# Performance work log

Measured on AMD Instinct MI355X. Metric: run time of the kernel, lower is better.

The kernel has to match this reference:

```python
import jax, jax.numpy as jnp
import numpy as np

N = 100000
E = 1600000
D = 128
H = 128


def gcn_conv(x, W, b, src, dst, n_nodes):
    # x: [N, Din] -> linear transform first (PyG GCNConv)
    h = x @ W  # [N, Dout]
    # add self loops
    loop = jnp.arange(n_nodes, dtype=src.dtype)
    s = jnp.concatenate([src, loop])
    d = jnp.concatenate([dst, loop])
    # symmetric normalization: deg computed on destination (col) with unit weights
    deg = jnp.zeros((n_nodes,), dtype=h.dtype).at[d].add(1.0)
    dinv = jnp.where(deg > 0, jax.lax.rsqrt(deg), 0.0)
    norm = dinv[s] * dinv[d]  # [E+N]
    msg = h[s] * norm[:, None]  # gather + scale
    out = jax.ops.segment_sum(msg, d, num_segments=n_nodes)
    return out + b


def setup_inputs() -> dict:
    key = jax.random.key(0)
    ks = jax.random.split(key, 8)
    x = jax.random.normal(ks[0], (N, D), dtype=jnp.float32)
    edge_index = jax.random.randint(ks[1], (2, E), 0, N, dtype=jnp.int32)
    sc = 1.0 / np.sqrt(D)
    gate_W = jax.random.uniform(ks[2], (D, D), jnp.float32, -sc, sc)
    gate_b = jax.random.uniform(ks[3], (D,), jnp.float32, -sc, sc)
    W1 = jax.random.normal(ks[4], (D, H), dtype=jnp.float32) * sc
    b1 = jnp.zeros((H,), jnp.float32)
    W2 = jax.random.normal(ks[5], (H, H), dtype=jnp.float32) * (1.0 / np.sqrt(H))
    b2 = jnp.zeros((H,), jnp.float32)
    return {"x": x, "edge_index": edge_index, "gate_W": gate_W, "gate_b": gate_b,
            "W1": W1, "b1": b1, "W2": W2, "b2": b2}


def reference(x, edge_index, gate_W, gate_b, W1, b1, W2, b2):
    src, dst = edge_index[0], edge_index[1]
    gate = jax.nn.sigmoid(x @ gate_W + gate_b)
    h = x * gate
    h = gcn_conv(h, W1, b1, src, dst, N)
    h = jax.nn.relu(h)
    h = gcn_conv(h, W2, b2, src, dst, N)
    return h
```

## Files before the change

### kernel.cpp

```cpp
#include <hip/hip_runtime.h>
#include <hip/hip_bf16.h>
#include <math.h>


#define BUCKET_SHIFT 8
#define BUCKET_W 256
#define CAP 4864
#define NB_MAX 512
#define OSTRIDE 136

typedef __attribute__((ext_vector_type(8))) short bf16x8;
typedef __attribute__((ext_vector_type(4))) float f32x4;

__device__ __forceinline__ unsigned short f2bf(float x) {
    unsigned int u = __float_as_uint(x);
    unsigned int r = (u + 0x7FFFu + ((u >> 16) & 1u)) >> 16;
    return (unsigned short)r;
}
__device__ __forceinline__ float blo(unsigned int u) { return __uint_as_float(u << 16); }
__device__ __forceinline__ float bhi(unsigned int u) { return __uint_as_float(u & 0xFFFF0000u); }

__device__ __forceinline__ void cvt_hilo8(const float* v, bf16x8& hi, bf16x8& lo) {
#pragma unroll
    for (int j = 0; j < 8; j++) {
        unsigned short h = f2bf(v[j]);
        float hf = __uint_as_float((unsigned int)h << 16);
        hi[j] = (short)h;
        lo[j] = (short)f2bf(v[j] - hf);
    }
}

__device__ __forceinline__ f32x4 MF(bf16x8 a, bf16x8 b, f32x4 c) {
    return __builtin_amdgcn_mfma_f32_16x16x32_bf16(a, b, c, 0, 0, 0);
}

__global__ void partition_kernel(const int* __restrict__ src, const int* __restrict__ dst,
                                 int* __restrict__ bucketCursor, unsigned int* __restrict__ part,
                                 int E, int NB, int chunk) {
    __shared__ int hist[NB_MAX];
    __shared__ int basec[NB_MAX];
    int t = threadIdx.x;
    int b = blockIdx.x;
    int e0 = b * chunk;
    int e1 = min(E, e0 + chunk);

    for (int i = t; i < NB; i += 256) hist[i] = 0;
    __syncthreads();
    for (int e = e0 + t; e < e1; e += 256) {
        int bb = dst[e] >> BUCKET_SHIFT;
        atomicAdd(&hist[bb], 1);
    }
    __syncthreads();
    for (int i = t; i < NB; i += 256) {
        int c = hist[i];
        basec[i] = c ? atomicAdd(&bucketCursor[i], c) : 0;
    }
    __syncthreads();
    for (int i = t; i < NB; i += 256) hist[i] = 0;
    __syncthreads();
    for (int e = e0 + t; e < e1; e += 256) {
        int d = dst[e], s = src[e];
        int bb = d >> BUCKET_SHIFT;
        int r = atomicAdd(&hist[bb], 1);
        int pos = basec[bb] + r;
        if (pos < CAP)
            part[(size_t)bb * CAP + pos] = ((unsigned int)(d & (BUCKET_W - 1)) << 17) | (unsigned int)s;
    }
}

__global__ void bucket_scan_kernel(const int* __restrict__ bucketCursor,
                                   int* __restrict__ bucketBase, int NB) {
    __shared__ int sm[NB_MAX];
    int t = threadIdx.x;
    int v = (t < NB) ? min(bucketCursor[t], CAP) : 0;
    sm[t] = v;
    __syncthreads();
    for (int off = 1; off < NB_MAX; off <<= 1) {
        int a = (t >= off) ? sm[t - off] : 0;
        __syncthreads();
        sm[t] += a;
        __syncthreads();
    }
    if (t < NB) bucketBase[t + 1] = sm[t];
    if (t == 0) bucketBase[0] = 0;
}

__launch_bounds__(256, 2)
__global__ void bucket_fill_kernel(const unsigned int* __restrict__ part,
                                   const int* __restrict__ bucketBase,
                                   int* __restrict__ rowptr, float* __restrict__ dinv,
                                   int* __restrict__ col, int N) {
    __shared__ unsigned int eLDS[CAP];
    __shared__ int deg[BUCKET_W];
    __shared__ int cur[BUCKET_W];
    __shared__ int wsum[4];

    int b = blockIdx.x, t = threadIdx.x;
    int base = bucketBase[b];
    int cnt = bucketBase[b + 1] - base;

    for (int i = t; i < cnt; i += 256) eLDS[i] = part[(size_t)b * CAP + i];
    deg[t] = 0;
    __syncthreads();
    for (int i = t; i < cnt; i += 256) atomicAdd(&deg[eLDS[i] >> 17], 1);
    __syncthreads();

    int v = deg[t];
    int incl = v;
    int lane = t & 63, w = t >> 6;
    for (int off = 1; off < 64; off <<= 1) {
        int u = __shfl_up(incl, off, 64);
        if (lane >= off) incl += u;
    }
    if (lane == 63) wsum[w] = incl;
    __syncthreads();
    int add = 0;
#pragma unroll
    for (int j = 0; j < 4; j++) if (j < w) add += wsum[j];
    int excl = add + incl - v;
    cur[t] = excl;

    int gnode = b * BUCKET_W + t;
    if (gnode < N) {
        rowptr[gnode] = base + excl;
        dinv[gnode] = rsqrtf((float)(v + 1));
    }
    if (b == gridDim.x - 1 && t == 0) rowptr[N] = base + cnt;
    __syncthreads();

    for (int i = t; i < cnt; i += 256) {
        unsigned int ev = eLDS[i];
        int dl = ev >> 17;
        int p = atomicAdd(&cur[dl], 1);
        col[base + p] = (int)(ev & 0x1FFFFu);
    }
}

__global__ void prep_weights_kernel(const float* __restrict__ W0, const float* __restrict__ W1,
                                    const float* __restrict__ W2, uint4* __restrict__ img) {
    int idx = blockIdx.x * 256 + threadIdx.x;
    int c = idx & 127, kb = (idx >> 7) & 15, w = idx >> 11;
    const float* W = (w == 0) ? W0 : (w == 1) ? W1 : W2;
    bf16x8 hb;
#pragma unroll
    for (int j = 0; j < 8; j++) hb[j] = (short)f2bf(W[(size_t)(kb * 8 + j) * 128 + c]);
    img[w * 2048 + c * 16 + (kb ^ (c & 15))] = *(uint4*)&hb;
}

__global__ __launch_bounds__(512)
void gate_kernel(const float* __restrict__ x, const uint4* __restrict__ gimg,
                 const float* __restrict__ gate_b, unsigned short* __restrict__ hpack,
                 int n) {
    __shared__ uint4 Wl[2048];
    __shared__ unsigned short OutS[128 * OSTRIDE];

    int t = threadIdx.x;
    int lane = t & 63, wv = t >> 6;
    int blockRow = blockIdx.x * 128;

    for (int idx = t; idx < 2048; idx += 512) Wl[idx] = gimg[idx];

    bf16x8 Ahi[4], Alo[4];
    {
        int arow = blockRow + wv * 16 + (lane & 15);
        const float* ap = x + (size_t)min(arow, n - 1) * 128 + (lane >> 4) * 8;
#pragma unroll
        for (int s = 0; s < 4; s++) {
            float v[8];
            *(float4*)&v[0] = *(const float4*)&ap[s * 32];
            *(float4*)&v[4] = *(const float4*)&ap[s * 32 + 4];
            cvt_hilo8(v, Ahi[s], Alo[s]);
        }
    }
    __syncthreads();

    f32x4 acc[8];
#pragma unroll
    for (int nt = 0; nt < 8; nt++) acc[nt] = (f32x4)(0.f);
#pragma unroll
    for (int s = 0; s < 4; s++) {
        int kb = s * 4 + (lane >> 4);
#pragma unroll
        for (int nt = 0; nt < 8; nt++) {
            int c = nt * 16 + (lane & 15);
            bf16x8 bh = *(bf16x8*)&Wl[c * 16 + (kb ^ (lane & 15))];
            acc[nt] = MF(Ahi[s], bh, acc[nt]);
            acc[nt] = MF(Alo[s], bh, acc[nt]);
        }
    }

    int rl0 = wv * 16 + (lane >> 4) * 4;
#pragma unroll
    for (int nt = 0; nt < 8; nt++) {
        int c = nt * 16 + (lane & 15);
        float gb = gate_b[c];
#pragma unroll
        for (int r = 0; r < 4; r++) {
            int grow = min(blockRow + rl0 + r, n - 1);
            float xv = x[(size_t)grow * 128 + c];
            float hv = xv / (1.f + __expf(-(acc[nt][r] + gb)));
            OutS[(rl0 + r) * OSTRIDE + c] = f2bf(hv);
        }
    }
    __syncthreads();
    {
        int row = t >> 2;
        int c0 = (t & 3) * 32;
        int grow = blockRow + row;
        if (grow < n) {
#pragma unroll
            for (int j = 0; j < 4; j++) {
                uint4 v = *(uint4*)&OutS[row * OSTRIDE + c0 + j * 8];
                *(uint4*)&hpack[(size_t)grow * 128 + c0 + j * 8] = v;
            }
        }
    }
}

__global__ __launch_bounds__(512)
void gemm_bf16_kernel(const unsigned short* __restrict__ A, const uint4* __restrict__ wimg,
                      const float* __restrict__ dinv, unsigned short* __restrict__ g,
                      int n) {
    __shared__ uint4 Wl[2048];
    __shared__ unsigned short OutS[128 * OSTRIDE];

    int t = threadIdx.x;
    int lane = t & 63, wv = t >> 6;
    int blockRow = blockIdx.x * 128;

    for (int idx = t; idx < 2048; idx += 512) Wl[idx] = wimg[idx];

    bf16x8 Af[4];
    {
        int arow = blockRow + wv * 16 + (lane & 15);
        const uint4* ap = (const uint4*)(A + (size_t)min(arow, n - 1) * 128);
#pragma unroll
        for (int s = 0; s < 4; s++) {
            uint4 u = ap[(lane >> 4) + s * 4];
            Af[s] = *(bf16x8*)&u;
        }
    }
    __syncthreads();

    f32x4 acc[8];
#pragma unroll
    for (int nt = 0; nt < 8; nt++) acc[nt] = (f32x4)(0.f);
#pragma unroll
    for (int s = 0; s < 4; s++) {
        int kb = s * 4 + (lane >> 4);
#pragma unroll
        for (int nt = 0; nt < 8; nt++) {
            int c = nt * 16 + (lane & 15);
            bf16x8 bh = *(bf16x8*)&Wl[c * 16 + (kb ^ (lane & 15))];
            acc[nt] = MF(Af[s], bh, acc[nt]);
        }
    }

    int rl0 = wv * 16 + (lane >> 4) * 4;
    float di[4];
#pragma unroll
    for (int r = 0; r < 4; r++) di[r] = dinv[min(blockRow + rl0 + r, n - 1)];
#pragma unroll
    for (int nt = 0; nt < 8; nt++) {
        int c = nt * 16 + (lane & 15);
#pragma unroll
        for (int r = 0; r < 4; r++)
            OutS[(rl0 + r) * OSTRIDE + c] = f2bf(acc[nt][r] * di[r]);
    }
    __syncthreads();
    {
        int row = t >> 2;
        int c0 = (t & 3) * 32;
        int grow = blockRow + row;
        if (grow < n) {
#pragma unroll
            for (int j = 0; j < 4; j++) {
                uint4 v = *(uint4*)&OutS[row * OSTRIDE + c0 + j * 8];
                *(uint4*)&g[(size_t)grow * 128 + c0 + j * 8] = v;
            }
        }
    }
}

template <int RELU, int PACK>
__global__ void spmm_kernel(const uint4* __restrict__ g16, const int* __restrict__ rowptr,
                            const int* __restrict__ col, const float* __restrict__ dinv,
                            const float* __restrict__ bias, void* __restrict__ outv,
                            int n) {
    int grp = threadIdx.x >> 4;
    int i = blockIdx.x * 16 + grp;
    if (i >= n) return;
    int c = threadIdx.x & 15;

    float acc[8];
    uint4 sv = g16[(size_t)i * 16 + c];
    acc[0] = blo(sv.x); acc[1] = bhi(sv.x);
    acc[2] = blo(sv.y); acc[3] = bhi(sv.y);
    acc[4] = blo(sv.z); acc[5] = bhi(sv.z);
    acc[6] = blo(sv.w); acc[7] = bhi(sv.w);

    int e0 = rowptr[i], e1 = rowptr[i + 1];
    int e = e0;
    for (; e + 4 <= e1; e += 4) {
        int s0 = col[e], s1 = col[e + 1], s2 = col[e + 2], s3 = col[e + 3];
        uint4 v0 = g16[(size_t)s0 * 16 + c];
        uint4 v1 = g16[(size_t)s1 * 16 + c];
        uint4 v2 = g16[(size_t)s2 * 16 + c];
        uint4 v3 = g16[(size_t)s3 * 16 + c];
        acc[0] += (blo(v0.x) + blo(v1.x)) + (blo(v2.x) + blo(v3.x));
        acc[1] += (bhi(v0.x) + bhi(v1.x)) + (bhi(v2.x) + bhi(v3.x));
        acc[2] += (blo(v0.y) + blo(v1.y)) + (blo(v2.y) + blo(v3.y));
        acc[3] += (bhi(v0.y) + bhi(v1.y)) + (bhi(v2.y) + bhi(v3.y));
        acc[4] += (blo(v0.z) + blo(v1.z)) + (blo(v2.z) + blo(v3.z));
        acc[5] += (bhi(v0.z) + bhi(v1.z)) + (bhi(v2.z) + bhi(v3.z));
        acc[6] += (blo(v0.w) + blo(v1.w)) + (blo(v2.w) + blo(v3.w));
        acc[7] += (bhi(v0.w) + bhi(v1.w)) + (bhi(v2.w) + bhi(v3.w));
    }
    for (; e < e1; e++) {
        int s0 = col[e];
        uint4 v0 = g16[(size_t)s0 * 16 + c];
        acc[0] += blo(v0.x); acc[1] += bhi(v0.x);
        acc[2] += blo(v0.y); acc[3] += bhi(v0.y);
        acc[4] += blo(v0.z); acc[5] += bhi(v0.z);
        acc[6] += blo(v0.w); acc[7] += bhi(v0.w);
    }

    float di = dinv[i];
    const float4* b4 = (const float4*)bias;
    float4 bv0 = b4[c * 2], bv1 = b4[c * 2 + 1];
    float r0[8];
    r0[0] = fmaf(acc[0], di, bv0.x);
    r0[1] = fmaf(acc[1], di, bv0.y);
    r0[2] = fmaf(acc[2], di, bv0.z);
    r0[3] = fmaf(acc[3], di, bv0.w);
    r0[4] = fmaf(acc[4], di, bv1.x);
    r0[5] = fmaf(acc[5], di, bv1.y);
    r0[6] = fmaf(acc[6], di, bv1.z);
    r0[7] = fmaf(acc[7], di, bv1.w);
    if (RELU) {
#pragma unroll
        for (int j = 0; j < 8; j++) r0[j] = fmaxf(r0[j], 0.f);
    }
    if (PACK) {
        ushort4 q0, q1;
        q0.x = f2bf(r0[0]); q0.y = f2bf(r0[1]); q0.z = f2bf(r0[2]); q0.w = f2bf(r0[3]);
        q1.x = f2bf(r0[4]); q1.y = f2bf(r0[5]); q1.z = f2bf(r0[6]); q1.w = f2bf(r0[7]);
        unsigned short* o = (unsigned short*)outv + (size_t)i * 128 + c * 8;
        *(ushort4*)&o[0] = q0;
        *(ushort4*)&o[4] = q1;
    } else {
        float* o = (float*)outv + (size_t)i * 128 + c * 8;
        *(float4*)&o[0] = *(float4*)&r0[0];
        *(float4*)&o[4] = *(float4*)&r0[4];
    }
}

extern "C" void kernel_launch(void* const* d_in, const int* in_sizes, int n_in,
                              void* d_out, int out_size, void* d_ws, size_t ws_size,
                              hipStream_t stream) {
    const float* x      = (const float*)d_in[0];
    const int*   ei     = (const int*)d_in[1];
    const float* gate_W = (const float*)d_in[2];
    const float* gate_b = (const float*)d_in[3];
    const float* W1     = (const float*)d_in[4];
    const float* b1     = (const float*)d_in[5];
    const float* W2     = (const float*)d_in[6];
    const float* b2     = (const float*)d_in[7];
    float* out = (float*)d_out;

    const int N = in_sizes[0] / 128;
    const int E = in_sizes[1] / 2;
    const int* src = ei;
    const int* dst = ei + E;
    const int NB = (N + BUCKET_W - 1) / BUCKET_W;

    char* p = (char*)d_ws;
    auto alloc = [&](size_t bytes) { char* q = p; p += (bytes + 255) & ~(size_t)255; return q; };
    int*   rowptr  = (int*)alloc(((size_t)N + 1) * 4);
    float* dinv    = (float*)alloc((size_t)N * 4);
    int*   colb    = (int*)alloc((size_t)E * 4);
    int*   bcursor = (int*)alloc((size_t)NB * 4);
    int*   bbase   = (int*)alloc(((size_t)NB + 1) * 4);
    uint4* wimg    = (uint4*)alloc((size_t)3 * 2048 * 16);
    unsigned int*   part    = (unsigned int*)alloc((size_t)NB * CAP * 4);
    unsigned short* hpack   = (unsigned short*)alloc((size_t)N * 128 * 2);
    unsigned short* g16     = (unsigned short*)alloc((size_t)N * 128 * 2);
    unsigned short* h1pack  = (unsigned short*)alloc((size_t)N * 128 * 2);

    prep_weights_kernel<<<24, 256, 0, stream>>>(gate_W, W1, W2, wimg);
    hipMemsetAsync(bcursor, 0, (size_t)NB * 4, stream);
    const int pblocks = 256;
    const int chunk = (E + pblocks - 1) / pblocks;
    partition_kernel<<<pblocks, 256, 0, stream>>>(src, dst, bcursor, part, E, NB, chunk);
    bucket_scan_kernel<<<1, NB_MAX, 0, stream>>>(bcursor, bbase, NB);
    bucket_fill_kernel<<<NB, 256, 0, stream>>>(part, bbase, rowptr, dinv, colb, N);

    int gblocks = (N + 127) / 128;
    int sblocks = (N + 15) / 16;
    gate_kernel<<<gblocks, 512, 0, stream>>>(x, wimg, gate_b, hpack, N);
    gemm_bf16_kernel<<<gblocks, 512, 0, stream>>>(hpack, wimg + 2048, dinv, g16, N);
    spmm_kernel<1, 1><<<sblocks, 256, 0, stream>>>((const uint4*)g16, rowptr, colb,
                                                   dinv, b1, h1pack, N);
    gemm_bf16_kernel<<<gblocks, 512, 0, stream>>>(h1pack, wimg + 4096, dinv, g16, N);
    spmm_kernel<0, 0><<<sblocks, 256, 0, stream>>>((const uint4*)g16, rowptr, colb,
                                                   dinv, b2, out, N);
}
```

Before: 245.6 us.

## Fuse graph-build stages with dense GEMMs and split SpMM columns into halves

Merges independent stages into shared launches. Weight prep and the cursor zeroing become one kernel, partition runs alongside the gate GEMM in one grid, and bucket fill runs alongside the first GCN GEMM in one grid. To allow that overlap, the first GEMM no longer applies dinv, and the first SpMM multiplies by dinv[src] per edge instead. Both SpMMs now split the 128 feature columns into two 64-column halves handled by separate blocks, and the final output uses nontemporal stores. This cuts launch count and serialisation, and lets graph construction overlap with dense work, at the cost of extra per-edge dinv loads and larger 512-thread blocks in the fill stage.

```diff
diff --git a/kernel.cpp b/kernel.cpp
--- a/kernel.cpp
+++ b/kernel.cpp
@@ -34,31 +34,50 @@
     return __builtin_amdgcn_mfma_f32_16x16x32_bf16(a, b, c, 0, 0, 0);
 }
 
-__global__ void partition_kernel(const int* __restrict__ src, const int* __restrict__ dst,
-                                 int* __restrict__ bucketCursor, unsigned int* __restrict__ part,
-                                 int E, int NB, int chunk) {
-    __shared__ int hist[NB_MAX];
-    __shared__ int basec[NB_MAX];
-    int t = threadIdx.x;
-    int b = blockIdx.x;
+__global__ __launch_bounds__(512)
+void prepinit_kernel(const float* __restrict__ W0, const float* __restrict__ W1,
+                     const float* __restrict__ W2, uint4* __restrict__ img,
+                     int* __restrict__ bcursor, int NB) {
+    int b = blockIdx.x, t = threadIdx.x;
+    if (b < 12) {
+        int idx = b * 512 + t;
+        int c = idx & 127, kb = (idx >> 7) & 15, w = idx >> 11;
+        const float* W = (w == 0) ? W0 : (w == 1) ? W1 : W2;
+        bf16x8 hb;
+#pragma unroll
+        for (int j = 0; j < 8; j++) hb[j] = (short)f2bf(W[(size_t)(kb * 8 + j) * 128 + c]);
+        img[w * 2048 + c * 16 + (kb ^ (c & 15))] = *(uint4*)&hb;
+    } else {
+        if (t < NB) bcursor[t] = 0;
+    }
+}
+
+__device__ __forceinline__ void partition_body(char* smem, int b, int t,
+                                               const int* __restrict__ src,
+                                               const int* __restrict__ dst,
+                                               int* __restrict__ bucketCursor,
+                                               unsigned int* __restrict__ part,
+                                               int E, int NB, int chunk) {
+    int* hist  = (int*)smem;
+    int* basec = hist + NB_MAX;
     int e0 = b * chunk;
     int e1 = min(E, e0 + chunk);
 
-    for (int i = t; i < NB; i += 256) hist[i] = 0;
-    __syncthreads();
-    for (int e = e0 + t; e < e1; e += 256) {
+    for (int i = t; i < NB; i += 512) hist[i] = 0;
+    __syncthreads();
+    for (int e = e0 + t; e < e1; e += 512) {
         int bb = dst[e] >> BUCKET_SHIFT;
         atomicAdd(&hist[bb], 1);
     }
     __syncthreads();
-    for (int i = t; i < NB; i += 256) {
+    for (int i = t; i < NB; i += 512) {
         int c = hist[i];
         basec[i] = c ? atomicAdd(&bucketCursor[i], c) : 0;
     }
     __syncthreads();
-    for (int i = t; i < NB; i += 256) hist[i] = 0;
-    __syncthreads();
-    for (int e = e0 + t; e < e1; e += 256) {
+    for (int i = t; i < NB; i += 512) hist[i] = 0;
+    __syncthreads();
+    for (int e = e0 + t; e < e1; e += 512) {
         int d = dst[e], s = src[e];
         int bb = d >> BUCKET_SHIFT;
         int r = atomicAdd(&hist[bb], 1);
@@ -68,8 +87,90 @@
     }
 }
 
-__global__ void bucket_scan_kernel(const int* __restrict__ bucketCursor,
-                                   int* __restrict__ bucketBase, int NB) {
+__device__ __forceinline__ void gate_body(char* smem, int gb, int t,
+                                          const float* __restrict__ x,
+                                          const uint4* __restrict__ gimg,
+                                          const float* __restrict__ gate_b,
+                                          unsigned short* __restrict__ hpack, int n) {
+    uint4* Wl = (uint4*)smem;
+    unsigned short* OutS = (unsigned short*)(smem + 32768);
+    int lane = t & 63, wv = t >> 6;
+    int blockRow = gb * 128;
+
+    for (int idx = t; idx < 2048; idx += 512) Wl[idx] = gimg[idx];
+
+    bf16x8 Ahi[4], Alo[4];
+    {
+        int arow = blockRow + wv * 16 + (lane & 15);
+        const float* ap = x + (size_t)min(arow, n - 1) * 128 + (lane >> 4) * 8;
+#pragma unroll
+        for (int s = 0; s < 4; s++) {
+            float v[8];
+            *(float4*)&v[0] = *(const float4*)&ap[s * 32];
+            *(float4*)&v[4] = *(const float4*)&ap[s * 32 + 4];
+            cvt_hilo8(v, Ahi[s], Alo[s]);
+        }
+    }
+    __syncthreads();
+
+    f32x4 acc[8];
+#pragma unroll
+    for (int nt = 0; nt < 8; nt++) acc[nt] = (f32x4)(0.f);
+#pragma unroll
+    for (int s = 0; s < 4; s++) {
+        int kb = s * 4 + (lane >> 4);
+#pragma unroll
+        for (int nt = 0; nt < 8; nt++) {
+            int c = nt * 16 + (lane & 15);
+            bf16x8 bh = *(bf16x8*)&Wl[c * 16 + (kb ^ (lane & 15))];
+            acc[nt] = MF(Ahi[s], bh, acc[nt]);
+            acc[nt] = MF(Alo[s], bh, acc[nt]);
+        }
+    }
+
+    int rl0 = wv * 16 + (lane >> 4) * 4;
+#pragma unroll
+    for (int nt = 0; nt < 8; nt++) {
+        int c = nt * 16 + (lane & 15);
+        float gb2 = gate_b[c];
+#pragma unroll
+        for (int r = 0; r < 4; r++) {
+            int grow = min(blockRow + rl0 + r, n - 1);
+            float xv = x[(size_t)grow * 128 + c];
+            float hv = xv / (1.f + __expf(-(acc[nt][r] + gb2)));
+            OutS[(rl0 + r) * OSTRIDE + c] = f2bf(hv);
+        }
+    }
+    __syncthreads();
+    {
+        int row = t >> 2;
+        int c0 = (t & 3) * 32;
+        int grow = blockRow + row;
+        if (grow < n) {
+#pragma unroll
+            for (int j = 0; j < 4; j++) {
+                uint4 v = *(uint4*)&OutS[row * OSTRIDE + c0 + j * 8];
+                *(uint4*)&hpack[(size_t)grow * 128 + c0 + j * 8] = v;
+            }
+        }
+    }
+}
+
+__global__ __launch_bounds__(512)
+void pg_kernel(const int* __restrict__ src, const int* __restrict__ dst,
+               int* __restrict__ bucketCursor, unsigned int* __restrict__ part,
+               int E, int NB, int chunk,
+               const float* __restrict__ x, const uint4* __restrict__ gimg,
+               const float* __restrict__ gate_b, unsigned short* __restrict__ hpack, int n) {
+    __shared__ __align__(16) char smem[67584];
+    int b = blockIdx.x, t = threadIdx.x;
+    if (b < 256) partition_body(smem, b, t, src, dst, bucketCursor, part, E, NB, chunk);
+    else         gate_body(smem, b - 256, t, x, gimg, gate_b, hpack, n);
+}
+
+__global__ __launch_bounds__(512)
+void bucket_scan_kernel(const int* __restrict__ bucketCursor,
+                        int* __restrict__ bucketBase, int NB) {
     __shared__ int sm[NB_MAX];
     int t = threadIdx.x;
     int v = (t < NB) ? min(bucketCursor[t], CAP) : 0;
@@ -85,27 +186,26 @@
     if (t == 0) bucketBase[0] = 0;
 }
 
-__launch_bounds__(256, 2)
-__global__ void bucket_fill_kernel(const unsigned int* __restrict__ part,
-                                   const int* __restrict__ bucketBase,
-                                   int* __restrict__ rowptr, float* __restrict__ dinv,
-                                   int* __restrict__ col, int N) {
-    __shared__ unsigned int eLDS[CAP];
-    __shared__ int deg[BUCKET_W];
-    __shared__ int cur[BUCKET_W];
-    __shared__ int wsum[4];
-
-    int b = blockIdx.x, t = threadIdx.x;
+__device__ __forceinline__ void fill_body(char* smem, int b, int t,
+                                          const unsigned int* __restrict__ part,
+                                          const int* __restrict__ bucketBase,
+                                          int* __restrict__ rowptr, float* __restrict__ dinv,
+                                          int* __restrict__ col, int N, int NB) {
+    unsigned int* eLDS = (unsigned int*)smem;
+    int* deg  = (int*)(smem + CAP * 4);
+    int* cur  = deg + BUCKET_W;
+    int* wsum = cur + BUCKET_W;
+
     int base = bucketBase[b];
     int cnt = bucketBase[b + 1] - base;
 
-    for (int i = t; i < cnt; i += 256) eLDS[i] = part[(size_t)b * CAP + i];
-    deg[t] = 0;
-    __syncthreads();
-    for (int i = t; i < cnt; i += 256) atomicAdd(&deg[eLDS[i] >> 17], 1);
-    __syncthreads();
-
-    int v = deg[t];
+    for (int i = t; i < cnt; i += 512) eLDS[i] = part[(size_t)b * CAP + i];
+    if (t < 256) deg[t] = 0;
+    __syncthreads();
+    for (int i = t; i < cnt; i += 512) atomicAdd(&deg[eLDS[i] >> 17], 1);
+    __syncthreads();
+
+    int v = (t < 256) ? deg[t] : 0;
     int incl = v;
     int lane = t & 63, w = t >> 6;
     for (int off = 1; off < 64; off <<= 1) {
@@ -118,17 +218,18 @@
 #pragma unroll
     for (int j = 0; j < 4; j++) if (j < w) add += wsum[j];
     int excl = add + incl - v;
-    cur[t] = excl;
-
-    int gnode = b * BUCKET_W + t;
-    if (gnode < N) {
-        rowptr[gnode] = base + excl;
-        dinv[gnode] = rsqrtf((float)(v + 1));
-    }
-    if (b == gridDim.x - 1 && t == 0) rowptr[N] = base + cnt;
-    __syncthreads();
-
-    for (int i = t; i < cnt; i += 256) {
+    if (t < 256) {
+        cur[t] = excl;
+        int gnode = b * BUCKET_W + t;
+        if (gnode < N) {
+            rowptr[gnode] = base + excl;
+            dinv[gnode] = rsqrtf((float)(v + 1));
+        }
+    }
+    if (b == NB - 1 && t == 0) rowptr[N] = base + cnt;
+    __syncthreads();
+
+    for (int i = t; i < cnt; i += 512) {
         unsigned int ev = eLDS[i];
         int dl = ev >> 17;
         int p = atomicAdd(&cur[dl], 1);
@@ -136,40 +237,27 @@
     }
 }
 
-__global__ void prep_weights_kernel(const float* __restrict__ W0, const float* __restrict__ W1,
-                                    const float* __restrict__ W2, uint4* __restrict__ img) {
-    int idx = blockIdx.x * 256 + threadIdx.x;
-    int c = idx & 127, kb = (idx >> 7) & 15, w = idx >> 11;
-    const float* W = (w == 0) ? W0 : (w == 1) ? W1 : W2;
-    bf16x8 hb;
-#pragma unroll
-    for (int j = 0; j < 8; j++) hb[j] = (short)f2bf(W[(size_t)(kb * 8 + j) * 128 + c]);
-    img[w * 2048 + c * 16 + (kb ^ (c & 15))] = *(uint4*)&hb;
-}
-
-__global__ __launch_bounds__(512)
-void gate_kernel(const float* __restrict__ x, const uint4* __restrict__ gimg,
-                 const float* __restrict__ gate_b, unsigned short* __restrict__ hpack,
-                 int n) {
-    __shared__ uint4 Wl[2048];
-    __shared__ unsigned short OutS[128 * OSTRIDE];
-
-    int t = threadIdx.x;
+template <int SCALE>
+__device__ __forceinline__ void gemm_body(char* smem, int gb, int t,
+                                          const unsigned short* __restrict__ A,
+                                          const uint4* __restrict__ wimg,
+                                          const float* __restrict__ dinv,
+                                          unsigned short* __restrict__ g, int n) {
+    uint4* Wl = (uint4*)smem;
+    unsigned short* OutS = (unsigned short*)(smem + 32768);
     int lane = t & 63, wv = t >> 6;
-    int blockRow = blockIdx.x * 128;
-
-    for (int idx = t; idx < 2048; idx += 512) Wl[idx] = gimg[idx];
-
-    bf16x8 Ahi[4], Alo[4];
+    int blockRow = gb * 128;
+
+    for (int idx = t; idx < 2048; idx += 512) Wl[idx] = wimg[idx];
+
+    bf16x8 Af[4];
     {
         int arow = blockRow + wv * 16 + (lane & 15);
-        const float* ap = x + (size_t)min(arow, n - 1) * 128 + (lane >> 4) * 8;
+        const uint4* ap = (const uint4*)(A + (size_t)min(arow, n - 1) * 128);
 #pragma unroll
         for (int s = 0; s < 4; s++) {
-            float v[8];
-            *(float4*)&v[0] = *(const float4*)&ap[s * 32];
-            *(float4*)&v[4] = *(const float4*)&ap[s * 32 + 4];
-            cvt_hilo8(v, Ahi[s], Alo[s]);
+            uint4 u = ap[(lane >> 4) + s * 4];
+            Af[s] = *(bf16x8*)&u;
         }
     }
     __syncthreads();
@@ -184,23 +272,21 @@
         for (int nt = 0; nt < 8; nt++) {
             int c = nt * 16 + (lane & 15);
             bf16x8 bh = *(bf16x8*)&Wl[c * 16 + (kb ^ (lane & 15))];
-            acc[nt] = MF(Ahi[s], bh, acc[nt]);
-            acc[nt] = MF(Alo[s], bh, acc[nt]);
+            acc[nt] = MF(Af[s], bh, acc[nt]);
         }
     }
 
     int rl0 = wv * 16 + (lane >> 4) * 4;
+    float di[4];
+#pragma unroll
+    for (int r = 0; r < 4; r++)
+        di[r] = SCALE ? dinv[min(blockRow + rl0 + r, n - 1)] : 1.f;
 #pragma unroll
     for (int nt = 0; nt < 8; nt++) {
         int c = nt * 16 + (lane & 15);
-        float gb = gate_b[c];
-#pragma unroll
-        for (int r = 0; r < 4; r++) {
-            int grow = min(blockRow + rl0 + r, n - 1);
-            float xv = x[(size_t)grow * 128 + c];
-            float hv = xv / (1.f + __expf(-(acc[nt][r] + gb)));
-            OutS[(rl0 + r) * OSTRIDE + c] = f2bf(hv);
-        }
+#pragma unroll
+        for (int r = 0; r < 4; r++)
+            OutS[(rl0 + r) * OSTRIDE + c] = f2bf(acc[nt][r] * di[r]);
     }
     __syncthreads();
     {
@@ -211,122 +297,84 @@
 #pragma unroll
             for (int j = 0; j < 4; j++) {
                 uint4 v = *(uint4*)&OutS[row * OSTRIDE + c0 + j * 8];
-                *(uint4*)&hpack[(size_t)grow * 128 + c0 + j * 8] = v;
+                *(uint4*)&g[(size_t)grow * 128 + c0 + j * 8] = v;
             }
         }
     }
+}
+
+__global__ __launch_bounds__(512)
+void fg_kernel(const unsigned int* __restrict__ part, const int* __restrict__ bucketBase,
+               int* __restrict__ rowptr, float* __restrict__ dinv, int* __restrict__ col,
+               int N, int NB,
+               const unsigned short* __restrict__ A, const uint4* __restrict__ wimg,
+               unsigned short* __restrict__ g) {
+    __shared__ __align__(16) char smem[67584];
+    int b = blockIdx.x, t = threadIdx.x;
+    if (b < NB) fill_body(smem, b, t, part, bucketBase, rowptr, dinv, col, N, NB);
+    else        gemm_body<0>(smem, b - NB, t, A, wimg, (const float*)nullptr, g, N);
 }
 
 __global__ __launch_bounds__(512)
 void gemm_bf16_kernel(const unsigned short* __restrict__ A, const uint4* __restrict__ wimg,
-                      const float* __restrict__ dinv, unsigned short* __restrict__ g,
-                      int n) {
-    __shared__ uint4 Wl[2048];
-    __shared__ unsigned short OutS[128 * OSTRIDE];
-
-    int t = threadIdx.x;
-    int lane = t & 63, wv = t >> 6;
-    int blockRow = blockIdx.x * 128;
-
-    for (int idx = t; idx < 2048; idx += 512) Wl[idx] = wimg[idx];
-
-    bf16x8 Af[4];
-    {
-        int arow = blockRow + wv * 16 + (lane & 15);
-        const uint4* ap = (const uint4*)(A + (size_t)min(arow, n - 1) * 128);
-#pragma unroll
-        for (int s = 0; s < 4; s++) {
-            uint4 u = ap[(lane >> 4) + s * 4];
-            Af[s] = *(bf16x8*)&u;
-        }
-    }
-    __syncthreads();
-
-    f32x4 acc[8];
-#pragma unroll
-    for (int nt = 0; nt < 8; nt++) acc[nt] = (f32x4)(0.f);
-#pragma unroll
-    for (int s = 0; s < 4; s++) {
-        int kb = s * 4 + (lane >> 4);
-#pragma unroll
-        for (int nt = 0; nt < 8; nt++) {
-            int c = nt * 16 + (lane & 15);
-            bf16x8 bh = *(bf16x8*)&Wl[c * 16 + (kb ^ (lane & 15))];
-            acc[nt] = MF(Af[s], bh, acc[nt]);
-        }
-    }
-
-    int rl0 = wv * 16 + (lane >> 4) * 4;
-    float di[4];
-#pragma unroll
-    for (int r = 0; r < 4; r++) di[r] = dinv[min(blockRow + rl0 + r, n - 1)];
-#pragma unroll
-    for (int nt = 0; nt < 8; nt++) {
-        int c = nt * 16 + (lane & 15);
-#pragma unroll
-        for (int r = 0; r < 4; r++)
-            OutS[(rl0 + r) * OSTRIDE + c] = f2bf(acc[nt][r] * di[r]);
-    }
-    __syncthreads();
-    {
-        int row = t >> 2;
-        int c0 = (t & 3) * 32;
-        int grow = blockRow + row;
-        if (grow < n) {
-#pragma unroll
-            for (int j = 0; j < 4; j++) {
-                uint4 v = *(uint4*)&OutS[row * OSTRIDE + c0 + j * 8];
-                *(uint4*)&g[(size_t)grow * 128 + c0 + j * 8] = v;
-            }
-        }
-    }
-}
-
-template <int RELU, int PACK>
+                      const float* __restrict__ dinv, unsigned short* __restrict__ g, int n) {
+    __shared__ __align__(16) char smem[67584];
+    gemm_body<1>(smem, blockIdx.x, threadIdx.x, A, wimg, dinv, g, n);
+}
+
+template <int RELU, int PACK, int DVSRC>
 __global__ void spmm_kernel(const uint4* __restrict__ g16, const int* __restrict__ rowptr,
                             const int* __restrict__ col, const float* __restrict__ dinv,
                             const float* __restrict__ bias, void* __restrict__ outv,
-                            int n) {
-    int grp = threadIdx.x >> 4;
-    int i = blockIdx.x * 16 + grp;
+                            int n, int nhb) {
+    int half = (blockIdx.x >= nhb) ? 1 : 0;
+    int rb = blockIdx.x - half * nhb;
+    int i = rb * 32 + (threadIdx.x >> 3);
     if (i >= n) return;
-    int c = threadIdx.x & 15;
-
+    int c = threadIdx.x & 7;
+
+    float di = dinv[i];
+    const uint4* gp = g16 + half * 8 + c;
     float acc[8];
-    uint4 sv = g16[(size_t)i * 16 + c];
-    acc[0] = blo(sv.x); acc[1] = bhi(sv.x);
-    acc[2] = blo(sv.y); acc[3] = bhi(sv.y);
-    acc[4] = blo(sv.z); acc[5] = bhi(sv.z);
-    acc[6] = blo(sv.w); acc[7] = bhi(sv.w);
+    uint4 sv = gp[(size_t)i * 16];
+    float wi = DVSRC ? di : 1.f;
+    acc[0] = wi * blo(sv.x); acc[1] = wi * bhi(sv.x);
+    acc[2] = wi * blo(sv.y); acc[3] = wi * bhi(sv.y);
+    acc[4] = wi * blo(sv.z); acc[5] = wi * bhi(sv.z);
+    acc[6] = wi * blo(sv.w); acc[7] = wi * bhi(sv.w);
 
     int e0 = rowptr[i], e1 = rowptr[i + 1];
     int e = e0;
     for (; e + 4 <= e1; e += 4) {
         int s0 = col[e], s1 = col[e + 1], s2 = col[e + 2], s3 = col[e + 3];
-        uint4 v0 = g16[(size_t)s0 * 16 + c];
-        uint4 v1 = g16[(size_t)s1 * 16 + c];
-        uint4 v2 = g16[(size_t)s2 * 16 + c];
-        uint4 v3 = g16[(size_t)s3 * 16 + c];
-        acc[0] += (blo(v0.x) + blo(v1.x)) + (blo(v2.x) + blo(v3.x));
-        acc[1] += (bhi(v0.x) + bhi(v1.x)) + (bhi(v2.x) + bhi(v3.x));
-        acc[2] += (blo(v0.y) + blo(v1.y)) + (blo(v2.y) + blo(v3.y));
-        acc[3] += (bhi(v0.y) + bhi(v1.y)) + (bhi(v2.y) + bhi(v3.y));
-        acc[4] += (blo(v0.z) + blo(v1.z)) + (blo(v2.z) + blo(v3.z));
-        acc[5] += (bhi(v0.z) + bhi(v1.z)) + (bhi(v2.z) + bhi(v3.z));
-        acc[6] += (blo(v0.w) + blo(v1.w)) + (blo(v2.w) + blo(v3.w));
-        acc[7] += (bhi(v0.w) + bhi(v1.w)) + (bhi(v2.w) + bhi(v3.w));
+        uint4 v0 = gp[(size_t)s0 * 16];
+        uint4 v1 = gp[(size_t)s1 * 16];
+        uint4 v2 = gp[(size_t)s2 * 16];
+        uint4 v3 = gp[(size_t)s3 * 16];
+        float w0 = DVSRC ? dinv[s0] : 1.f;
+        float w1 = DVSRC ? dinv[s1] : 1.f;
+        float w2 = DVSRC ? dinv[s2] : 1.f;
+        float w3 = DVSRC ? dinv[s3] : 1.f;
+        acc[0] = fmaf(w0, blo(v0.x), fmaf(w1, blo(v1.x), fmaf(w2, blo(v2.x), fmaf(w3, blo(v3.x), acc[0]))));
+        acc[1] = fmaf(w0, bhi(v0.x), fmaf(w1, bhi(v1.x), fmaf(w2, bhi(v2.x), fmaf(w3, bhi(v3.x), acc[1]))));
+        acc[2] = fmaf(w0, blo(v0.y), fmaf(w1, blo(v1.y), fmaf(w2, blo(v2.y), fmaf(w3, blo(v3.y), acc[2]))));
+        acc[3] = fmaf(w0, bhi(v0.y), fmaf(w1, bhi(v1.y), fmaf(w2, bhi(v2.y), fmaf(w3, bhi(v3.y), acc[3]))));
+        acc[4] = fmaf(w0, blo(v0.z), fmaf(w1, blo(v1.z), fmaf(w2, blo(v2.z), fmaf(w3, blo(v3.z), acc[4]))));
+        acc[5] = fmaf(w0, bhi(v0.z), fmaf(w1, bhi(v1.z), fmaf(w2, bhi(v2.z), fmaf(w3, bhi(v3.z), acc[5]))));
+        acc[6] = fmaf(w0, blo(v0.w), fmaf(w1, blo(v1.w), fmaf(w2, blo(v2.w), fmaf(w3, blo(v3.w), acc[6]))));
+        acc[7] = fmaf(w0, bhi(v0.w), fmaf(w1, bhi(v1.w), fmaf(w2, bhi(v2.w), fmaf(w3, bhi(v3.w), acc[7]))));
     }
     for (; e < e1; e++) {
         int s0 = col[e];
-        uint4 v0 = g16[(size_t)s0 * 16 + c];
-        acc[0] += blo(v0.x); acc[1] += bhi(v0.x);
-        acc[2] += blo(v0.y); acc[3] += bhi(v0.y);
-        acc[4] += blo(v0.z); acc[5] += bhi(v0.z);
-        acc[6] += blo(v0.w); acc[7] += bhi(v0.w);
-    }
-
-    float di = dinv[i];
-    const float4* b4 = (const float4*)bias;
+        uint4 v0 = gp[(size_t)s0 * 16];
+        float w0 = DVSRC ? dinv[s0] : 1.f;
+        acc[0] = fmaf(w0, blo(v0.x), acc[0]); acc[1] = fmaf(w0, bhi(v0.x), acc[1]);
+        acc[2] = fmaf(w0, blo(v0.y), acc[2]); acc[3] = fmaf(w0, bhi(v0.y), acc[3]);
+        acc[4] = fmaf(w0, blo(v0.z), acc[4]); acc[5] = fmaf(w0, bhi(v0.z), acc[5]);
+        acc[6] = fmaf(w0, blo(v0.w), acc[6]); acc[7] = fmaf(w0, bhi(v0.w), acc[7]);
+    }
+
+    const float4* b4 = (const float4*)(bias + half * 64);
     float4 bv0 = b4[c * 2], bv1 = b4[c * 2 + 1];
     float r0[8];
     r0[0] = fmaf(acc[0], di, bv0.x);
@@ -342,16 +390,18 @@
         for (int j = 0; j < 8; j++) r0[j] = fmaxf(r0[j], 0.f);
     }
     if (PACK) {
-        ushort4 q0, q1;
-        q0.x = f2bf(r0[0]); q0.y = f2bf(r0[1]); q0.z = f2bf(r0[2]); q0.w = f2bf(r0[3]);
-        q1.x = f2bf(r0[4]); q1.y = f2bf(r0[5]); q1.z = f2bf(r0[6]); q1.w = f2bf(r0[7]);
-        unsigned short* o = (unsigned short*)outv + (size_t)i * 128 + c * 8;
-        *(ushort4*)&o[0] = q0;
-        *(ushort4*)&o[4] = q1;
+        uint4 w;
+        w.x = (unsigned int)f2bf(r0[0]) | ((unsigned int)f2bf(r0[1]) << 16);
+        w.y = (unsigned int)f2bf(r0[2]) | ((unsigned int)f2bf(r0[3]) << 16);
+        w.z = (unsigned int)f2bf(r0[4]) | ((unsigned int)f2bf(r0[5]) << 16);
+        w.w = (unsigned int)f2bf(r0[6]) | ((unsigned int)f2bf(r0[7]) << 16);
+        *(uint4*)((unsigned short*)outv + (size_t)i * 128 + half * 64 + c * 8) = w;
     } else {
-        float* o = (float*)outv + (size_t)i * 128 + c * 8;
-        *(float4*)&o[0] = *(float4*)&r0[0];
-        *(float4*)&o[4] = *(float4*)&r0[4];
+        float* o = (float*)outv + (size_t)i * 128 + half * 64 + c * 8;
+        f32x4 a = *(f32x4*)&r0[0];
+        f32x4 b = *(f32x4*)&r0[4];
+        __builtin_nontemporal_store(a, (f32x4*)o);
+        __builtin_nontemporal_store(b, (f32x4*)(o + 4));
     }
 }
 
@@ -382,26 +432,25 @@
     int*   bcursor = (int*)alloc((size_t)NB * 4);
     int*   bbase   = (int*)alloc(((size_t)NB + 1) * 4);
     uint4* wimg    = (uint4*)alloc((size_t)3 * 2048 * 16);
-    unsigned int*   part    = (unsigned int*)alloc((size_t)NB * CAP * 4);
-    unsigned short* hpack   = (unsigned short*)alloc((size_t)N * 128 * 2);
-    unsigned short* g16     = (unsigned short*)alloc((size_t)N * 128 * 2);
-    unsigned short* h1pack  = (unsigned short*)alloc((size_t)N * 128 * 2);
-
-    prep_weights_kernel<<<24, 256, 0, stream>>>(gate_W, W1, W2, wimg);
-    hipMemsetAsync(bcursor, 0, (size_t)NB * 4, stream);
+    unsigned int*   part   = (unsigned int*)alloc((size_t)NB * CAP * 4);
+    unsigned short* hpack  = (unsigned short*)alloc((size_t)N * 128 * 2);
+    unsigned short* g16    = (unsigned short*)alloc((size_t)N * 128 * 2);
+    unsigned short* h1pack = (unsigned short*)alloc((size_t)N * 128 * 2);
+
     const int pblocks = 256;
     const int chunk = (E + pblocks - 1) / pblocks;
-    partition_kernel<<<pblocks, 256, 0, stream>>>(src, dst, bcursor, part, E, NB, chunk);
-    bucket_scan_kernel<<<1, NB_MAX, 0, stream>>>(bcursor, bbase, NB);
-    bucket_fill_kernel<<<NB, 256, 0, stream>>>(part, bbase, rowptr, dinv, colb, N);
-
     int gblocks = (N + 127) / 128;
-    int sblocks = (N + 15) / 16;
-    gate_kernel<<<gblocks, 512, 0, stream>>>(x, wimg, gate_b, hpack, N);
-    gemm_bf16_kernel<<<gblocks, 512, 0, stream>>>(hpack, wimg + 2048, dinv, g16, N);
-    spmm_kernel<1, 1><<<sblocks, 256, 0, stream>>>((const uint4*)g16, rowptr, colb,
-                                                   dinv, b1, h1pack, N);
+    int nhb = (N + 31) / 32;
+
+    prepinit_kernel<<<13, 512, 0, stream>>>(gate_W, W1, W2, wimg, bcursor, NB);
+    pg_kernel<<<256 + gblocks, 512, 0, stream>>>(src, dst, bcursor, part, E, NB, chunk,
+                                                 x, wimg, gate_b, hpack, N);
+    bucket_scan_kernel<<<1, 512, 0, stream>>>(bcursor, bbase, NB);
+    fg_kernel<<<NB + gblocks, 512, 0, stream>>>(part, bbase, rowptr, dinv, colb, N, NB,
+                                                hpack, wimg + 2048, g16);
+    spmm_kernel<1, 1, 1><<<2 * nhb, 256, 0, stream>>>((const uint4*)g16, rowptr, colb,
+                                                      dinv, b1, h1pack, N, nhb);
     gemm_bf16_kernel<<<gblocks, 512, 0, stream>>>(h1pack, wimg + 4096, dinv, g16, N);
-    spmm_kernel<0, 0><<<sblocks, 256, 0, stream>>>((const uint4*)g16, rowptr, colb,
-                                                   dinv, b2, out, N);
-}
+    spmm_kernel<0, 0, 0><<<2 * nhb, 256, 0, stream>>>((const uint4*)g16, rowptr, colb,
+                                                      dinv, b2, out, N, nhb);
+}
```

Result: faster. 215.6 us (-12.2%).
